# Kernel optimization log

Measured on AMD Instinct MI355X. Metric: run time of the kernel, lower is better.

The kernel has to match this reference:

```python
import jax, jax.numpy as jnp
import numpy as np

S, B, C = 7, 2, 20
LC, LN = 5.0, 0.5  # lambda_coord, lambda_noobj
CELL = 1.0 / S


def _iou(b1, b2):
    # center (x, y, w, h) boxes, broadcastable [..., 4]
    x1a, y1a = b1[..., 0] - b1[..., 2] / 2, b1[..., 1] - b1[..., 3] / 2
    x2a, y2a = b1[..., 0] + b1[..., 2] / 2, b1[..., 1] + b1[..., 3] / 2
    x1b, y1b = b2[..., 0] - b2[..., 2] / 2, b2[..., 1] - b2[..., 3] / 2
    x2b, y2b = b2[..., 0] + b2[..., 2] / 2, b2[..., 1] + b2[..., 3] / 2
    iw = jnp.maximum(jnp.minimum(x2a, x2b) - jnp.maximum(x1a, x1b), 0.0)
    ih = jnp.maximum(jnp.minimum(y2a, y2b) - jnp.maximum(y1a, y1b), 0.0)
    inter = iw * ih
    union = b1[..., 2] * b1[..., 3] + b2[..., 2] * b2[..., 3] - inter
    return inter / jnp.maximum(union, 1e-10)


def setup_inputs() -> dict:
    key = jax.random.key(0)
    k1, k2, k3 = jax.random.split(key, 3)
    N, T = 16384, 16
    outputs = jax.random.normal(k1, (N, S, S, B * 5 + C), dtype=jnp.float32)
    # normalized xywh, kept strictly inside (0,1) so grid indices are valid
    boxes = jax.random.uniform(k2, (N, T, 4), dtype=jnp.float32, minval=0.01, maxval=0.99)
    labels = jax.random.randint(k3, (N, T), 1, C + 1)  # class labels in 1..C
    return {"outputs": outputs, "boxes": boxes, "labels": labels}


def reference(outputs, boxes, labels):
    N = outputs.shape[0]
    T = boxes.shape[1]
    bbox = outputs[..., : B * 5].reshape(N, S, S, B, 5)
    conf = bbox[..., 4]                         # [N,S,S,B]
    cls_logits = outputs[..., B * 5:]           # [N,S,S,C]
    # decode predicted centers to absolute image coords (as in the original)
    gx = jnp.arange(S, dtype=outputs.dtype)[None, :, None]  # column index
    gy = jnp.arange(S, dtype=outputs.dtype)[:, None, None]  # row index
    px = (bbox[..., 0] + gx) * CELL
    py = (bbox[..., 1] + gy) * CELL
    pred = jnp.stack([px, py, bbox[..., 2], bbox[..., 3]], axis=-1)  # [N,S,S,B,4]

    tx, ty, tw, th = boxes[..., 0], boxes[..., 1], boxes[..., 2], boxes[..., 3]  # [N,T]
    gxi = (tx * S).astype(jnp.int32)
    gyi = (ty * S).astype(jnp.int32)
    offx = tx * S - gxi.astype(tx.dtype)
    offy = ty * S - gyi.astype(ty.dtype)

    bi = jnp.arange(N)[:, None]  # [N,1] broadcasts with [N,T]
    cell_pred = pred[bi, gyi, gxi]          # [N,T,B,4]
    cell_conf = conf[bi, gyi, gxi]          # [N,T,B]
    cell_cls = cls_logits[bi, gyi, gxi]     # [N,T,C]

    ious = _iou(boxes[:, :, None, :], cell_pred)   # [N,T,B]
    best = (B - 1) - jnp.argmax(ious[..., ::-1], axis=-1)  # [N,T]

    bp = jnp.take_along_axis(cell_pred, best[:, :, None, None], axis=2)[:, :, 0, :]  # [N,T,4]
    bconf = jnp.take_along_axis(cell_conf, best[:, :, None], axis=2)[:, :, 0]        # [N,T]

    eps = 1e-6
    box_loss = (
        (bp[..., 0] - offx) ** 2
        + (bp[..., 1] - offy) ** 2
        + (jnp.sqrt(jnp.maximum(bp[..., 2], eps)) - jnp.sqrt(jnp.maximum(tw, eps))) ** 2
        + (jnp.sqrt(jnp.maximum(bp[..., 3], eps)) - jnp.sqrt(jnp.maximum(th, eps))) ** 2
    ).sum(axis=-1)                                     # [N]
    obj_loss = ((bconf - 1.0) ** 2).sum(axis=-1)        # [N]

    probs = jax.nn.softmax(cell_cls, axis=-1)           # [N,T,C]
    onehot = jax.nn.one_hot(labels - 1, C, dtype=probs.dtype)
    class_loss = ((probs - onehot) ** 2).sum(axis=-1).sum(axis=-1)  # [N]

    obj_mask = jnp.zeros((N, S, S, B), dtype=bool).at[bi, gyi, gxi, best].set(True)
    nm = ~obj_mask
    cnt = nm.sum(axis=(1, 2, 3)).astype(conf.dtype)     # always > 0 (T < S*S*B)
    noobj_loss = (conf ** 2 * nm).sum(axis=(1, 2, 3)) / cnt  # mean over unmasked conf

    per_img = LC * box_loss + class_loss + obj_loss + LN * noobj_loss
    return per_img.mean()
```

## Files before the change

kernel.cpp:

```cpp
#include <hip/hip_runtime.h>

#define NCH   30
#define NCONF 98
#define IMGF  1470
#define LCf 5.0f
#define LNf 0.5f

#define AS1 __attribute__((address_space(1)))
#define AS3 __attribute__((address_space(3)))

__device__ __forceinline__ float img_partial(const float* __restrict__ img,
                                             float4 bx, int lab,
                                             volatile unsigned char* sm,
                                             int lane, int t, int q, float cf1)
{
    float ns = cf1 * cf1;
    if (lane < NCONF - 64) {
        int s2 = lane + 64;
        int c2 = s2 >> 1, b2 = s2 & 1;
        float cf2 = img[c2 * NCH + b2 * 5 + 4];
        ns += cf2 * cf2;
    }

    const float tx = bx.x, ty = bx.y, tw = bx.z, th = bx.w;
    const float fx = tx * 7.0f, fy = ty * 7.0f;
    const int gxi = (int)fx, gyi = (int)fy;
    const float offx = fx - (float)gxi;
    const float offy = fy - (float)gyi;
    const int cellIdx = gyi * 7 + gxi;
    const float* cell = img + cellIdx * NCH;

    float px = 0.f, py = 0.f, pw = 0.f, ph = 0.f, pc = 0.f, iou_own = 0.f;
    if (q < 2) {
        float rx = cell[q * 5 + 0];
        float ry = cell[q * 5 + 1];
        pw       = cell[q * 5 + 2];
        ph       = cell[q * 5 + 3];
        pc       = cell[q * 5 + 4];
        px = (rx + (float)gxi) * (1.0f / 7.0f);
        py = (ry + (float)gyi) * (1.0f / 7.0f);

        float x1a = tx - tw * 0.5f, y1a = ty - th * 0.5f;
        float x2a = tx + tw * 0.5f, y2a = ty + th * 0.5f;
        float x1b = px - pw * 0.5f, y1b = py - ph * 0.5f;
        float x2b = px + pw * 0.5f, y2b = py + ph * 0.5f;
        float iw = fmaxf(fminf(x2a, x2b) - fmaxf(x1a, x1b), 0.0f);
        float ih = fmaxf(fminf(y2a, y2b) - fmaxf(y1a, y1b), 0.0f);
        float inter = iw * ih;
        float uni = tw * th + pw * ph - inter;
        iou_own = inter / fmaxf(uni, 1e-10f);
    }
    const float iou_other = __shfl_xor(iou_own, 1);
    int bestq = 0;
    if (q < 2) {
        float i0 = (q == 0) ? iou_own   : iou_other;
        float i1 = (q == 0) ? iou_other : iou_own;
        bestq = (i1 >= i0) ? 1 : 0;
    }
    const int best = __shfl(bestq, lane & ~3);
    const int s = cellIdx * 2 + best;

    float contrib = 0.0f;
    const float eps = 1e-6f;
    if (q == best) {
        float dx = px - offx, dy = py - offy;
        float dw = sqrtf(fmaxf(pw, eps)) - sqrtf(fmaxf(tw, eps));
        float dh = sqrtf(fmaxf(ph, eps)) - sqrtf(fmaxf(th, eps));
        float box_l = dx * dx + dy * dy + dw * dw + dh * dh;
        float obj_l = (pc - 1.0f) * (pc - 1.0f);
        contrib = LCf * box_l + obj_l;
    }

    if (q == best) sm[s] = (unsigned char)lane;
    asm volatile("s_waitcnt lgkmcnt(0)" ::: "memory");
    __builtin_amdgcn_sched_barrier(0);
    const bool winner = (q == best) && (sm[s] == (unsigned char)lane);
    const unsigned long long bal = __ballot(winner);
    const int mc = __popcll(bal);
    const float ms = winner ? pc * pc : 0.0f;

    {
        float cv[5];
        #pragma unroll
        for (int i = 0; i < 5; ++i) cv[i] = cell[10 + q * 5 + i];
        float m = fmaxf(fmaxf(fmaxf(cv[0], cv[1]), fmaxf(cv[2], cv[3])), cv[4]);
        m = fmaxf(m, __shfl_xor(m, 1));
        m = fmaxf(m, __shfl_xor(m, 2));
        float esum = 0.f, e2 = 0.f, elab = 0.f;
        #pragma unroll
        for (int i = 0; i < 5; ++i) {
            float e = __expf(cv[i] - m);
            esum += e; e2 += e * e;
            if (q * 5 + i == lab) elab = e;
        }
        esum += __shfl_xor(esum, 1);  esum += __shfl_xor(esum, 2);
        e2   += __shfl_xor(e2,   1);  e2   += __shfl_xor(e2,   2);
        elab += __shfl_xor(elab, 1);  elab += __shfl_xor(elab, 2);
        if (q == 0) {
            float inv = 1.0f / esum;
            contrib += e2 * inv * inv - 2.0f * elab * inv + 1.0f;
        }
    }

    const float invDen = 1.0f / (98.0f - (float)mc);
    return contrib + LNf * (ns - ms) * invDen;
}

__global__ __launch_bounds__(256) void yolo_loss_kernel(
    const float* __restrict__ outputs,
    const float* __restrict__ boxes,
    const int*   __restrict__ labels,
    float*       __restrict__ block_sum)
{
    const int tid  = threadIdx.x;
    const int wave = tid >> 6;
    const int lane = tid & 63;
    const int t    = lane >> 2;
    const int q    = lane & 3;
    const int n    = blockIdx.x * 4 + wave;

    __shared__ float         s_img[4 * IMGF];
    __shared__ unsigned char s_m[4][112];
    __shared__ float         s_ws[4];

    const float4 bx = reinterpret_cast<const float4*>(boxes)[(size_t)n * 16 + t];
    const int   lab = labels[(size_t)n * 16 + t] - 1;

    const float* gsrc = outputs + (size_t)n * IMGF;
    char* wbase = (char*)&s_img[wave * IMGF];
    const int odd = wave & 1;
    {
        const float* sgp = odd ? gsrc : (gsrc + IMGF - 2);
        char*        slp = odd ? wbase : (wbase + (size_t)(IMGF - 2) * 4);
        if (lane < 2) {
            __builtin_amdgcn_global_load_lds((const AS1 void*)(sgp + lane),
                                             (AS3 void*)slp, 4, 0, 0);
        }
        const float4* g4 = reinterpret_cast<const float4*>(gsrc + (odd ? 2 : 0));
        char* l4 = wbase + (odd ? 8 : 0);
        #pragma unroll
        for (int k = 0; k < 5; ++k) {
            __builtin_amdgcn_global_load_lds(
                (const AS1 void*)(g4 + k * 64 + lane),
                (AS3 void*)(l4 + (size_t)k * 1024), 16, 0, 0);
        }
        if (lane < 367 - 320) {
            __builtin_amdgcn_global_load_lds(
                (const AS1 void*)(g4 + 320 + lane),
                (AS3 void*)(l4 + (size_t)5 * 1024), 16, 0, 0);
        }
    }

    const float* img = &s_img[wave * IMGF];

    asm volatile("s_waitcnt vmcnt(2)" ::: "memory");
    __builtin_amdgcn_sched_barrier(0);
    const float cf1 = img[(lane >> 1) * NCH + (lane & 1) * 5 + 4];

    asm volatile("s_waitcnt vmcnt(0)" ::: "memory");
    __builtin_amdgcn_sched_barrier(0);

    float v = img_partial(img, bx, lab, s_m[wave], lane, t, q, cf1);

    #pragma unroll
    for (int off = 32; off > 0; off >>= 1) v += __shfl_xor(v, off);
    if (lane == 0) s_ws[wave] = v;
    __syncthreads();
    if (tid == 0)
        block_sum[blockIdx.x] = (s_ws[0] + s_ws[1]) + (s_ws[2] + s_ws[3]);
}

__global__ __launch_bounds__(256) void reduce_mean_kernel(
    const float* __restrict__ block_sum, float* __restrict__ out, int nb, int N)
{
    __shared__ double sd[4];
    double acc = 0.0;
    const float4* p4 = reinterpret_cast<const float4*>(block_sum);
    for (int i = threadIdx.x; i < nb / 4; i += 256) {
        float4 v = p4[i];
        acc += (double)v.x + (double)v.y + (double)v.z + (double)v.w;
    }
    #pragma unroll
    for (int off = 32; off > 0; off >>= 1) acc += __shfl_xor(acc, off);
    if ((threadIdx.x & 63) == 0) sd[threadIdx.x >> 6] = acc;
    __syncthreads();
    if (threadIdx.x == 0)
        out[0] = (float)(((sd[0] + sd[1]) + (sd[2] + sd[3])) / (double)N);
}

extern "C" void kernel_launch(void* const* d_in, const int* in_sizes, int n_in,
                              void* d_out, int out_size, void* d_ws, size_t ws_size,
                              hipStream_t stream) {
    const float* outputs = (const float*)d_in[0];
    const float* boxes   = (const float*)d_in[1];
    const int*   labels  = (const int*)d_in[2];
    float* out = (float*)d_out;

    const int N  = in_sizes[0] / IMGF;
    const int nb = N / 4;
    float* block_sum = (float*)d_ws;

    yolo_loss_kernel<<<nb, 256, 0, stream>>>(outputs, boxes, labels, block_sum);
    reduce_mean_kernel<<<1, 256, 0, stream>>>(block_sum, out, nb, N);
}
```

Measured before the change: 24.26 us.

## Use DPP lane ops, 2-wave blocks, per-image sums with wider final reduction

Replaces ds_bpermute-based shuffles with DPP quad-permute and row-rotate ops plus readlane for the intra-wave reductions. Shrinks blocks from 4 to 2 waves, which halves LDS per block and removes the block-level __syncthreads. Each wave now writes its own per-image sum, and the final reduction kernel grows to 1024 threads to consume four times as many partials. The goal is lower shuffle latency and finer-grained scheduling, at the cost of a larger second-stage reduction and more blocks.

```diff
diff --git a/kernel.cpp b/kernel.cpp
--- a/kernel.cpp
+++ b/kernel.cpp
@@ -8,6 +8,21 @@
 
 #define AS1 __attribute__((address_space(1)))
 #define AS3 __attribute__((address_space(3)))
+
+template<int CTRL>
+__device__ __forceinline__ float dppf(float v) {
+    return __int_as_float(__builtin_amdgcn_update_dpp(
+        0, __float_as_int(v), CTRL, 0xF, 0xF, true));
+}
+#define QP_XOR1 0xB1
+#define QP_XOR2 0x4E
+#define QP_B0   0x00
+#define ROW_ROR4 0x124
+#define ROW_ROR8 0x128
+
+__device__ __forceinline__ float rlane(float v, int k) {
+    return __int_as_float(__builtin_amdgcn_readlane(__float_as_int(v), k));
+}
 
 __device__ __forceinline__ float img_partial(const float* __restrict__ img,
                                              float4 bx, int lab,
@@ -50,14 +65,14 @@
         float uni = tw * th + pw * ph - inter;
         iou_own = inter / fmaxf(uni, 1e-10f);
     }
-    const float iou_other = __shfl_xor(iou_own, 1);
+    const float iou_other = dppf<QP_XOR1>(iou_own);
     int bestq = 0;
     if (q < 2) {
         float i0 = (q == 0) ? iou_own   : iou_other;
         float i1 = (q == 0) ? iou_other : iou_own;
         bestq = (i1 >= i0) ? 1 : 0;
     }
-    const int best = __shfl(bestq, lane & ~3);
+    const int best = __builtin_amdgcn_update_dpp(0, bestq, QP_B0, 0xF, 0xF, true);
     const int s = cellIdx * 2 + best;
 
     float contrib = 0.0f;
@@ -84,8 +99,8 @@
         #pragma unroll
         for (int i = 0; i < 5; ++i) cv[i] = cell[10 + q * 5 + i];
         float m = fmaxf(fmaxf(fmaxf(cv[0], cv[1]), fmaxf(cv[2], cv[3])), cv[4]);
-        m = fmaxf(m, __shfl_xor(m, 1));
-        m = fmaxf(m, __shfl_xor(m, 2));
+        m = fmaxf(m, dppf<QP_XOR1>(m));
+        m = fmaxf(m, dppf<QP_XOR2>(m));
         float esum = 0.f, e2 = 0.f, elab = 0.f;
         #pragma unroll
         for (int i = 0; i < 5; ++i) {
@@ -93,9 +108,9 @@
             esum += e; e2 += e * e;
             if (q * 5 + i == lab) elab = e;
         }
-        esum += __shfl_xor(esum, 1);  esum += __shfl_xor(esum, 2);
-        e2   += __shfl_xor(e2,   1);  e2   += __shfl_xor(e2,   2);
-        elab += __shfl_xor(elab, 1);  elab += __shfl_xor(elab, 2);
+        esum += dppf<QP_XOR1>(esum);  esum += dppf<QP_XOR2>(esum);
+        e2   += dppf<QP_XOR1>(e2);    e2   += dppf<QP_XOR2>(e2);
+        elab += dppf<QP_XOR1>(elab);  elab += dppf<QP_XOR2>(elab);
         if (q == 0) {
             float inv = 1.0f / esum;
             contrib += e2 * inv * inv - 2.0f * elab * inv + 1.0f;
@@ -106,22 +121,21 @@
     return contrib + LNf * (ns - ms) * invDen;
 }
 
-__global__ __launch_bounds__(256) void yolo_loss_kernel(
+__global__ __launch_bounds__(128) void yolo_loss_kernel(
     const float* __restrict__ outputs,
     const float* __restrict__ boxes,
     const int*   __restrict__ labels,
-    float*       __restrict__ block_sum)
+    float*       __restrict__ per_img)
 {
     const int tid  = threadIdx.x;
     const int wave = tid >> 6;
     const int lane = tid & 63;
     const int t    = lane >> 2;
     const int q    = lane & 3;
-    const int n    = blockIdx.x * 4 + wave;
-
-    __shared__ float         s_img[4 * IMGF];
-    __shared__ unsigned char s_m[4][112];
-    __shared__ float         s_ws[4];
+    const int n    = blockIdx.x * 2 + wave;
+
+    __shared__ __align__(16) float s_img[2 * IMGF];
+    __shared__ unsigned char       s_m[2][112];
 
     const float4 bx = reinterpret_cast<const float4*>(boxes)[(size_t)n * 16 + t];
     const int   lab = labels[(size_t)n * 16 + t] - 1;
@@ -162,21 +176,21 @@
 
     float v = img_partial(img, bx, lab, s_m[wave], lane, t, q, cf1);
 
-    #pragma unroll
-    for (int off = 32; off > 0; off >>= 1) v += __shfl_xor(v, off);
-    if (lane == 0) s_ws[wave] = v;
-    __syncthreads();
-    if (tid == 0)
-        block_sum[blockIdx.x] = (s_ws[0] + s_ws[1]) + (s_ws[2] + s_ws[3]);
-}
-
-__global__ __launch_bounds__(256) void reduce_mean_kernel(
-    const float* __restrict__ block_sum, float* __restrict__ out, int nb, int N)
+    v += dppf<QP_XOR1>(v);
+    v += dppf<QP_XOR2>(v);
+    v += dppf<ROW_ROR4>(v);
+    v += dppf<ROW_ROR8>(v);
+    const float tot = (rlane(v, 0) + rlane(v, 16)) + (rlane(v, 32) + rlane(v, 48));
+    if (lane == 0) per_img[n] = tot;
+}
+
+__global__ __launch_bounds__(1024) void reduce_mean_kernel(
+    const float* __restrict__ per_img, float* __restrict__ out, int N)
 {
-    __shared__ double sd[4];
+    __shared__ double sd[16];
     double acc = 0.0;
-    const float4* p4 = reinterpret_cast<const float4*>(block_sum);
-    for (int i = threadIdx.x; i < nb / 4; i += 256) {
+    const float4* p4 = reinterpret_cast<const float4*>(per_img);
+    for (int i = threadIdx.x; i < N / 4; i += 1024) {
         float4 v = p4[i];
         acc += (double)v.x + (double)v.y + (double)v.z + (double)v.w;
     }
@@ -184,8 +198,12 @@
     for (int off = 32; off > 0; off >>= 1) acc += __shfl_xor(acc, off);
     if ((threadIdx.x & 63) == 0) sd[threadIdx.x >> 6] = acc;
     __syncthreads();
-    if (threadIdx.x == 0)
-        out[0] = (float)(((sd[0] + sd[1]) + (sd[2] + sd[3])) / (double)N);
+    if (threadIdx.x == 0) {
+        double tsum = 0.0;
+        #pragma unroll
+        for (int w = 0; w < 16; ++w) tsum += sd[w];
+        out[0] = (float)(tsum / (double)N);
+    }
 }
 
 extern "C" void kernel_launch(void* const* d_in, const int* in_sizes, int n_in,
@@ -197,9 +215,9 @@
     float* out = (float*)d_out;
 
     const int N  = in_sizes[0] / IMGF;
-    const int nb = N / 4;
-    float* block_sum = (float*)d_ws;
-
-    yolo_loss_kernel<<<nb, 256, 0, stream>>>(outputs, boxes, labels, block_sum);
-    reduce_mean_kernel<<<1, 256, 0, stream>>>(block_sum, out, nb, N);
-}
+    const int nb = N / 2;
+    float* per_img = (float*)d_ws;
+
+    yolo_loss_kernel<<<nb, 128, 0, stream>>>(outputs, boxes, labels, per_img);
+    reduce_mean_kernel<<<1, 1024, 0, stream>>>(per_img, out, N);
+}
```

Measured after the change: 24.37 us, median of 2. Within noise of the previous version (+0.5%).
